# Kernel optimization log

Measured on AMD Instinct MI355X. Metric: run time of the kernel, lower is better.

Reference implementation:

```python
import jax, jax.numpy as jnp
import numpy as np

E, D, H, B, S = 16, 1024, 256, 4, 4096  # num_splats, model_dim, ff_dim//num_splats, batch, seq_len


def setup_inputs() -> dict:
    key = jax.random.key(0)
    ks = jax.random.split(key, 8)
    s = 0.02  # init scale for stability
    return {
        "x": jax.random.normal(ks[0], (B, S, D), dtype=jnp.float32),
        "splat_id": jax.random.randint(ks[1], (S,), 0, E, dtype=jnp.int32),
        "W1": jax.random.normal(ks[2], (E, D, H), dtype=jnp.float32) * s,
        "b1": jnp.zeros((E, H), dtype=jnp.float32),
        "W2": jax.random.normal(ks[3], (E, H, D), dtype=jnp.float32) * s,
        "b2": jnp.zeros((E, D), dtype=jnp.float32),
        "Wg1": jax.random.normal(ks[4], (D, D), dtype=jnp.float32) * s,
        "bg1": jnp.zeros((D,), dtype=jnp.float32),
        "Wg2": jax.random.normal(ks[5], (D, D), dtype=jnp.float32) * s,
        "bg2": jnp.zeros((D,), dtype=jnp.float32),
    }


def reference(x, splat_id, W1, b1, W2, b2, Wg1, bg1, Wg2, bg2):
    # Splat-aware dispatch: token s is processed by expert splat_id[s].
    # Equivalent vectorized form: run every expert's small MLP, mask at the
    # hidden layer by expert assignment, and sum over experts (each token is
    # assigned to exactly one expert, matching the gather->MLP->scatter loop).
    nE = W1.shape[0]
    onehot = (splat_id[None, :] == jnp.arange(nE, dtype=splat_id.dtype)[:, None]).astype(x.dtype)  # [E,S]
    # hidden: [E,B,S,H]
    h = jax.nn.gelu(jnp.einsum('bsd,edh->ebsh', x, W1) + b1[:, None, None, :], approximate=False)
    h = h * onehot[:, None, :, None]  # zero tokens not routed to expert e
    routed = jnp.einsum('ebsh,ehd->bsd', h, W2)  # [B,S,D]
    routed = routed + jnp.einsum('es,ed->sd', onehot, b2)[None, :, :]  # per-token expert bias
    # global aggregator MLP (torch GELU default = exact erf form)
    g = jax.nn.gelu(routed @ Wg1 + bg1, approximate=False)
    return g @ Wg2 + bg2
```

## Files before the change

### kernel.cpp

```cpp
#include <hip/hip_runtime.h>


#define DEV __device__ __forceinline__

typedef float f32x4 __attribute__((ext_vector_type(4)));
typedef short short8 __attribute__((ext_vector_type(8)));

DEV unsigned short f2bf(float f) {
  unsigned u = __float_as_uint(f);
  u += 0x7fffu + ((u >> 16) & 1u);
  return (unsigned short)(u >> 16);
}

DEV void gload16(const void* g, void* l) {
  __builtin_amdgcn_global_load_lds(
      (const __attribute__((address_space(1))) unsigned int*)g,
      (__attribute__((address_space(3))) unsigned int*)l, 16, 0, 0);
}

DEV float gelu_exact(float v) {
  return 0.5f * v * (1.0f + erff(v * 0.70710678118654752f));
}

__global__ __launch_bounds__(256) void prep_kernel(
    const float* __restrict__ W1, unsigned short* __restrict__ w1t,
    const float* __restrict__ W2, unsigned short* __restrict__ w2t,
    const float* __restrict__ Wg1, unsigned short* __restrict__ wg1t,
    const float* __restrict__ Wg2, unsigned short* __restrict__ wg2t) {
  __shared__ float tile[64][65];
  const int t = threadIdx.x;
  int id = (int)blockIdx.x;
  const float* in; unsigned short* out;
  int R, C, r0, c0; long base;
  if (id < 1024) {
    in = W1; out = w1t; R = 1024; C = 256;
    base = (long)(id >> 6) * 262144;
    r0 = ((id >> 2) & 15) * 64; c0 = (id & 3) * 64;
  } else if (id < 2048) {
    id -= 1024;
    in = W2; out = w2t; R = 256; C = 1024;
    base = (long)(id >> 6) * 262144;
    r0 = ((id >> 4) & 3) * 64; c0 = (id & 15) * 64;
  } else if (id < 2304) {
    id -= 2048;
    in = Wg1; out = wg1t; R = 1024; C = 1024; base = 0;
    r0 = (id >> 4) * 64; c0 = (id & 15) * 64;
  } else {
    id -= 2304;
    in = Wg2; out = wg2t; R = 1024; C = 1024; base = 0;
    r0 = (id >> 4) * 64; c0 = (id & 15) * 64;
  }
  const int cc = t & 63, rr = t >> 6;
#pragma unroll
  for (int i = 0; i < 16; i++) {
    int r = rr + i * 4;
    tile[r][cc] = in[base + (long)(r0 + r) * C + (c0 + cc)];
  }
  __syncthreads();
#pragma unroll
  for (int i = 0; i < 16; i++) {
    int c = rr + i * 4;
    out[base + (long)(c0 + c) * R + (r0 + cc)] = f2bf(tile[cc][c]);
  }
}

__global__ __launch_bounds__(256) void route_kernel(
    const int* __restrict__ sid, int S, int* __restrict__ offs, int* __restrict__ order,
    int* __restrict__ tileE, int* __restrict__ tileR, int* __restrict__ ntl,
    int* __restrict__ t64E, int* __restrict__ t64R, int* __restrict__ ntl64) {
  __shared__ int cnt[16], cur[16];
  const int t = threadIdx.x;
  if (t < 16) cnt[t] = 0;
  __syncthreads();
  for (int s = t; s < S; s += 256) atomicAdd(&cnt[sid[s]], 1);
  __syncthreads();
  if (t == 0) {
    int a = 0;
    for (int e = 0; e < 16; e++) { offs[e] = a; cur[e] = a; a += cnt[e]; }
    offs[16] = a;
    int nt = 0, n64 = 0;
    for (int e = 0; e < 16; e++) {
      const int rows = 4 * cnt[e];
      for (int r = 0; r < rows; r += 128) {
        tileE[nt] = e; tileR[nt] = 4 * offs[e] + r; nt++;
      }
      for (int r = 0; r < rows; r += 64) {
        t64E[n64] = e; t64R[n64] = 4 * offs[e] + r; n64++;
      }
    }
    ntl[0] = nt;
    ntl64[0] = n64;
  }
  __syncthreads();
  for (int s = t; s < S; s += 256) {
    int p = atomicAdd(&cur[sid[s]], 1);
    order[p] = s;
  }
}

__global__ __launch_bounds__(256, 4) void gemm_g1(
    const float* __restrict__ x,
    const unsigned short* __restrict__ w1t, const float* __restrict__ b1,
    unsigned short* __restrict__ hbuf,
    const int* __restrict__ order, const int* __restrict__ offs,
    const int* __restrict__ t64E, const int* __restrict__ t64R,
    const int* __restrict__ ntl64) {
  constexpr int S = 4096, D = 1024, H = 256;
  const int ti = (int)blockIdx.y;
  if (ti >= ntl64[0]) return;
  const int ntile = (int)blockIdx.x;
  const int t = (int)threadIdx.x;
  const int lane = t & 63;
  const int wn = t >> 6;

  const int e = t64E[ti];
  const int rowBase = t64R[ti];
  int Me = 4 * offs[e + 1] - rowBase;
  if (Me > 64) Me = 64;

  __shared__ __align__(16) unsigned short lA[64 * 64];
  __shared__ __align__(16) unsigned short lB[128 * 64];

  const float* xsrc[2];
  int aDst[2];
#pragma unroll
  for (int i = 0; i < 2; i++) {
    const int row = i * 32 + (t >> 3);
    const int koff = (((t & 7) * 16) ^ ((row & 7) << 4)) >> 1;
    const int rr = (row < Me) ? row : (Me - 1);
    const int g = rowBase + rr;
    xsrc[i] = x + ((long)(g & 3) * S + order[g >> 2]) * D + koff;
    aDst[i] = row * 64 + (t & 7) * 8;
  }
  const unsigned short* bSrc[4];
#pragma unroll
  for (int i = 0; i < 4; i++) {
    const int row = i * 32 + (t >> 3);
    bSrc[i] = w1t + (long)e * H * D + (long)(ntile * 128 + row) * D +
              ((((t & 7) * 16) ^ ((row & 7) << 4)) >> 1);
  }
  const int dstE = (t >> 3) * 64 + (t & 7) * 8;

  f32x4 acc[4][2] = {};
  float4 xv[2][2];
#pragma unroll
  for (int i = 0; i < 2; i++) {
    xv[i][0] = *(const float4*)(xsrc[i]);
    xv[i][1] = *(const float4*)(xsrc[i] + 4);
  }

  for (int kt = 0; kt < 16; kt++) {
    __syncthreads();
#pragma unroll
    for (int i = 0; i < 2; i++) {
      short8 av;
      av[0] = (short)f2bf(xv[i][0].x); av[1] = (short)f2bf(xv[i][0].y);
      av[2] = (short)f2bf(xv[i][0].z); av[3] = (short)f2bf(xv[i][0].w);
      av[4] = (short)f2bf(xv[i][1].x); av[5] = (short)f2bf(xv[i][1].y);
      av[6] = (short)f2bf(xv[i][1].z); av[7] = (short)f2bf(xv[i][1].w);
      *(short8*)(lA + aDst[i]) = av;
    }
#pragma unroll
    for (int i = 0; i < 4; i++)
      gload16(bSrc[i] + (kt << 6), lB + i * 2048 + dstE);
    if (kt < 15) {
#pragma unroll
      for (int i = 0; i < 2; i++) {
        xv[i][0] = *(const float4*)(xsrc[i] + (kt + 1) * 64);
        xv[i][1] = *(const float4*)(xsrc[i] + (kt + 1) * 64 + 4);
      }
    }
    __syncthreads();
#pragma unroll
    for (int kk = 0; kk < 2; kk++) {
      short8 aF[4], bF[2];
      const int kb = kk * 64 + ((lane >> 4) << 4);
#pragma unroll
      for (int mi = 0; mi < 4; mi++) {
        const int row = mi * 16 + (lane & 15);
        aF[mi] = *(const short8*)((const char*)lA + row * 128 + (kb ^ ((row & 7) << 4)));
      }
#pragma unroll
      for (int ni = 0; ni < 2; ni++) {
        const int row = wn * 32 + ni * 16 + (lane & 15);
        bF[ni] = *(const short8*)((const char*)lB + row * 128 + (kb ^ ((row & 7) << 4)));
      }
#pragma unroll
      for (int mi = 0; mi < 4; mi++)
#pragma unroll
        for (int ni = 0; ni < 2; ni++)
          acc[mi][ni] = __builtin_amdgcn_mfma_f32_16x16x32_bf16(aF[mi], bF[ni], acc[mi][ni], 0, 0, 0);
    }
  }

  float bc[2];
#pragma unroll
  for (int ni = 0; ni < 2; ni++)
    bc[ni] = b1[e * H + ntile * 128 + wn * 32 + ni * 16 + (lane & 15)];
#pragma unroll
  for (int mi = 0; mi < 4; mi++)
#pragma unroll
    for (int j = 0; j < 4; j++) {
      const int lrow = mi * 16 + ((lane >> 4) << 2) + j;
      if (lrow >= Me) continue;
      const long crow = rowBase + lrow;
#pragma unroll
      for (int ni = 0; ni < 2; ni++) {
        const float v = gelu_exact(acc[mi][ni][j] + bc[ni]);
        hbuf[crow * H + ntile * 128 + wn * 32 + ni * 16 + (lane & 15)] = f2bf(v);
      }
    }
}

__global__ __launch_bounds__(256) void gemm_g2(
    const unsigned short* __restrict__ A, const unsigned short* __restrict__ BT,
    const float* __restrict__ bias, unsigned short* __restrict__ Cout,
    int N, int K,
    const int* __restrict__ order, const int* __restrict__ offs,
    const int* __restrict__ tileE, const int* __restrict__ tileR,
    const int* __restrict__ ntl,
    int S, long btStride, int biasStride) {
  const int ti = (int)blockIdx.y;
  if (ti >= ntl[0]) return;
  const int t = (int)threadIdx.x;
  const int lane = t & 63;
  const int w = t >> 6;
  const int wm = w >> 1, wn = w & 1;
  const int tileN = (int)blockIdx.x;

  const int e = tileE[ti];
  const int rowBase = tileR[ti];
  int Me = 4 * offs[e + 1] - rowBase;
  if (Me > 128) Me = 128;
  const unsigned short* bt = BT + (long)e * btStride;
  const float* bs = bias + (long)e * biasStride;

  __shared__ __align__(16) unsigned short lA[128 * 64];
  __shared__ __align__(16) unsigned short lB[128 * 64];

  const unsigned short* aSrc[4];
  const unsigned short* bSrc[4];
  {
    const int q = t & 7;
#pragma unroll
    for (int i = 0; i < 4; i++) {
      const int row = i * 32 + (t >> 3);
      const int koff = ((q * 16) ^ ((row & 7) << 4)) >> 1;
      const int rr = (row < Me) ? row : (Me - 1);
      const int g = rowBase + rr;
      aSrc[i] = A + (long)g * K + koff;
      const int col = tileN * 128 + row;
      bSrc[i] = bt + (long)col * K + koff;
    }
  }

  f32x4 acc[4][4] = {};

  const int KT = K >> 6;
  for (int kt = 0; kt < KT; kt++) {
    __syncthreads();
#pragma unroll
    for (int i = 0; i < 4; i++) {
      gload16(aSrc[i] + (kt << 6), (void*)(lA + i * 2048 + w * 512));
      gload16(bSrc[i] + (kt << 6), (void*)(lB + i * 2048 + w * 512));
    }
    __syncthreads();
#pragma unroll
    for (int kk = 0; kk < 2; kk++) {
      short8 af[4], bfr[4];
      const int kbyte = kk * 64 + (lane >> 4) * 16;
#pragma unroll
      for (int mi = 0; mi < 4; mi++) {
        const int row = wm * 64 + mi * 16 + (lane & 15);
        const int off = row * 128 + (kbyte ^ ((row & 7) << 4));
        af[mi] = *(const short8*)((const char*)lA + off);
      }
#pragma unroll
      for (int ni = 0; ni < 4; ni++) {
        const int row = wn * 64 + ni * 16 + (lane & 15);
        const int off = row * 128 + (kbyte ^ ((row & 7) << 4));
        bfr[ni] = *(const short8*)((const char*)lB + off);
      }
#pragma unroll
      for (int mi = 0; mi < 4; mi++)
#pragma unroll
        for (int ni = 0; ni < 4; ni++)
          acc[mi][ni] = __builtin_amdgcn_mfma_f32_16x16x32_bf16(af[mi], bfr[ni], acc[mi][ni], 0, 0, 0);
    }
  }

  float bcol[4];
#pragma unroll
  for (int ni = 0; ni < 4; ni++)
    bcol[ni] = bs[tileN * 128 + wn * 64 + ni * 16 + (lane & 15)];

#pragma unroll
  for (int mi = 0; mi < 4; mi++) {
#pragma unroll
    for (int j = 0; j < 4; j++) {
      const int lrow = wm * 64 + mi * 16 + ((lane >> 4) * 4) + j;
      if (lrow >= Me) continue;
      const int g = rowBase + lrow;
      const long crow = (long)(g & 3) * S + order[g >> 2];
#pragma unroll
      for (int ni = 0; ni < 4; ni++) {
        const float v = acc[mi][ni][j] + bcol[ni];
        Cout[crow * (long)N + tileN * 128 + wn * 64 + ni * 16 + (lane & 15)] = f2bf(v);
      }
    }
  }
}

template <bool GELU, bool OUT_F32>
__global__ __launch_bounds__(256, 4) void gemm_dense128(
    const unsigned short* __restrict__ A, const unsigned short* __restrict__ BT,
    const float* __restrict__ bias, void* __restrict__ Cout,
    int N, int K, int ntiles) {
  const int t = (int)threadIdx.x;
  const int lane = t & 63;
  const int w = t >> 6;
  const int wm = w >> 1, wn = w & 1;

  const int cpx = (int)gridDim.x >> 3;
  const int swz = ((int)blockIdx.x & 7) * cpx + ((int)blockIdx.x >> 3);
  const int mtile = swz / ntiles, ntile = swz % ntiles;

  __shared__ __align__(16) unsigned short lA[128 * 64];
  __shared__ __align__(16) unsigned short lB[128 * 64];

  const unsigned short* aSrc[4];
  const unsigned short* bSrc[4];
  {
    const int q = t & 7;
#pragma unroll
    for (int i = 0; i < 4; i++) {
      const int row = i * 32 + (t >> 3);
      const int koff = ((q * 16) ^ ((row & 7) << 4)) >> 1;
      aSrc[i] = A + (long)(mtile * 128 + row) * K + koff;
      bSrc[i] = BT + (long)(ntile * 128 + row) * K + koff;
    }
  }

  f32x4 acc[4][4] = {};

  const int KT = K >> 6;
  for (int kt = 0; kt < KT; kt++) {
    __syncthreads();
#pragma unroll
    for (int i = 0; i < 4; i++) {
      gload16(aSrc[i] + (kt << 6), (void*)(lA + i * 2048 + w * 512));
      gload16(bSrc[i] + (kt << 6), (void*)(lB + i * 2048 + w * 512));
    }
    __syncthreads();
#pragma unroll
    for (int kk = 0; kk < 2; kk++) {
      short8 af[4], bfr[4];
      const int kbyte = kk * 64 + (lane >> 4) * 16;
#pragma unroll
      for (int mi = 0; mi < 4; mi++) {
        const int row = wm * 64 + mi * 16 + (lane & 15);
        const int off = row * 128 + (kbyte ^ ((row & 7) << 4));
        af[mi] = *(const short8*)((const char*)lA + off);
      }
#pragma unroll
      for (int ni = 0; ni < 4; ni++) {
        const int row = wn * 64 + ni * 16 + (lane & 15);
        const int off = row * 128 + (kbyte ^ ((row & 7) << 4));
        bfr[ni] = *(const short8*)((const char*)lB + off);
      }
#pragma unroll
      for (int mi = 0; mi < 4; mi++)
#pragma unroll
        for (int ni = 0; ni < 4; ni++)
          acc[mi][ni] = __builtin_amdgcn_mfma_f32_16x16x32_bf16(af[mi], bfr[ni], acc[mi][ni], 0, 0, 0);
    }
  }

  float bcol[4];
#pragma unroll
  for (int ni = 0; ni < 4; ni++)
    bcol[ni] = bias[ntile * 128 + wn * 64 + ni * 16 + (lane & 15)];

#pragma unroll
  for (int mi = 0; mi < 4; mi++) {
#pragma unroll
    for (int j = 0; j < 4; j++) {
      const long crow = mtile * 128 + wm * 64 + mi * 16 + ((lane >> 4) * 4) + j;
#pragma unroll
      for (int ni = 0; ni < 4; ni++) {
        float v = acc[mi][ni][j] + bcol[ni];
        if (GELU) v = gelu_exact(v);
        const long cidx = crow * (long)N + ntile * 128 + wn * 64 + ni * 16 + (lane & 15);
        if (OUT_F32) ((float*)Cout)[cidx] = v;
        else ((unsigned short*)Cout)[cidx] = f2bf(v);
      }
    }
  }
}

extern "C" void kernel_launch(void* const* d_in, const int* in_sizes, int n_in,
                              void* d_out, int out_size, void* d_ws, size_t ws_size,
                              hipStream_t stream) {
  const float* x   = (const float*)d_in[0];
  const int*   sid = (const int*)d_in[1];
  const float* W1  = (const float*)d_in[2];
  const float* b1  = (const float*)d_in[3];
  const float* W2  = (const float*)d_in[4];
  const float* b2  = (const float*)d_in[5];
  const float* Wg1 = (const float*)d_in[6];
  const float* bg1 = (const float*)d_in[7];
  const float* Wg2 = (const float*)d_in[8];
  const float* bg2 = (const float*)d_in[9];
  (void)in_sizes; (void)n_in; (void)out_size; (void)ws_size;

  constexpr int D = 1024, H = 256, S = 4096, B = 4;
  constexpr long NT = (long)B * S;

  char* ws = (char*)d_ws;
  unsigned short* gbuf = (unsigned short*)(ws);
  unsigned short* w1t  = (unsigned short*)(ws + 33554432);
  unsigned short* w2t  = (unsigned short*)(ws + 41943040);
  unsigned short* wg1t = (unsigned short*)(ws + 50331648);
  unsigned short* wg2t = (unsigned short*)(ws + 52428800);
  unsigned short* hbuf = (unsigned short*)(ws + 54525952);
  unsigned short* rout = (unsigned short*)(ws + 62914560);
  int* offs  = (int*)(ws + 96468992);
  int* order = (int*)(ws + 96469248);
  int* tileE = (int*)(ws + 96485632);
  int* tileR = (int*)(ws + 96486208);
  int* ntl   = (int*)(ws + 96486784);
  int* t64E  = (int*)(ws + 96487424);
  int* t64R  = (int*)(ws + 96488704);
  int* ntl64 = (int*)(ws + 96489984);

  prep_kernel<<<dim3(2560), 256, 0, stream>>>(W1, w1t, W2, w2t, Wg1, wg1t, Wg2, wg2t);
  route_kernel<<<1, 256, 0, stream>>>(sid, S, offs, order, tileE, tileR, ntl, t64E, t64R, ntl64);

  gemm_g1<<<dim3(H / 128, 272), 256, 0, stream>>>(
      x, w1t, b1, hbuf, order, offs, t64E, t64R, ntl64);
  gemm_g2<<<dim3(D / 128, 144), 256, 0, stream>>>(
      hbuf, w2t, b2, rout, D, H, order, offs, tileE, tileR, ntl, S, (long)D * H, D);
  gemm_dense128<true, false><<<dim3((unsigned)(NT / 128) * (D / 128)), 256, 0, stream>>>(
      rout, wg1t, bg1, gbuf, D, D, D / 128);
  gemm_dense128<false, true><<<dim3((unsigned)(NT / 128) * (D / 128)), 256, 0, stream>>>(
      gbuf, wg2t, bg2, d_out, D, D, D / 128);
}
```

Measured before the change: 181.3 us.

## Use 128-row tiles in expert GEMM1 with fp32 async LDS loads of x

Expert GEMM1 moves from 64x128 tiles to 128x128 tiles over a 2x2 wave grid, so each block reuses weight tiles across twice as many token rows and the grid has half as many row tiles. The gathered fp32 activations now go straight into LDS through async global_load_lds instead of through registers with an explicit bf16 convert-and-store. Conversion to bf16 happens while reading LDS fragments, using round-half-up rather than round-to-nearest-even. This doubles the A-tile LDS footprint and the accumulator registers (occupancy hint lowered to 3), and drops the register prefetch of the next x tile. Launch bounds on gemm_g2 and the launch order of the route and prep kernels also change.

```diff
diff --git a/kernel.cpp b/kernel.cpp
--- a/kernel.cpp
+++ b/kernel.cpp
@@ -20,6 +20,35 @@
 
 DEV float gelu_exact(float v) {
   return 0.5f * v * (1.0f + erff(v * 0.70710678118654752f));
+}
+
+__global__ __launch_bounds__(256) void route_kernel(
+    const int* __restrict__ sid, int S, int* __restrict__ offs, int* __restrict__ order,
+    int* __restrict__ tileE, int* __restrict__ tileR, int* __restrict__ ntl) {
+  __shared__ int cnt[16], cur[16];
+  const int t = threadIdx.x;
+  if (t < 16) cnt[t] = 0;
+  __syncthreads();
+  for (int s = t; s < S; s += 256) atomicAdd(&cnt[sid[s]], 1);
+  __syncthreads();
+  if (t == 0) {
+    int a = 0;
+    for (int e = 0; e < 16; e++) { offs[e] = a; cur[e] = a; a += cnt[e]; }
+    offs[16] = a;
+    int nt = 0;
+    for (int e = 0; e < 16; e++) {
+      const int rows = 4 * cnt[e];
+      for (int r = 0; r < rows; r += 128) {
+        tileE[nt] = e; tileR[nt] = 4 * offs[e] + r; nt++;
+      }
+    }
+    ntl[0] = nt;
+  }
+  __syncthreads();
+  for (int s = t; s < S; s += 256) {
+    int p = atomicAdd(&cur[sid[s]], 1);
+    order[p] = s;
+  }
 }
 
 __global__ __launch_bounds__(256) void prep_kernel(
@@ -64,74 +93,41 @@
   }
 }
 
-__global__ __launch_bounds__(256) void route_kernel(
-    const int* __restrict__ sid, int S, int* __restrict__ offs, int* __restrict__ order,
-    int* __restrict__ tileE, int* __restrict__ tileR, int* __restrict__ ntl,
-    int* __restrict__ t64E, int* __restrict__ t64R, int* __restrict__ ntl64) {
-  __shared__ int cnt[16], cur[16];
-  const int t = threadIdx.x;
-  if (t < 16) cnt[t] = 0;
-  __syncthreads();
-  for (int s = t; s < S; s += 256) atomicAdd(&cnt[sid[s]], 1);
-  __syncthreads();
-  if (t == 0) {
-    int a = 0;
-    for (int e = 0; e < 16; e++) { offs[e] = a; cur[e] = a; a += cnt[e]; }
-    offs[16] = a;
-    int nt = 0, n64 = 0;
-    for (int e = 0; e < 16; e++) {
-      const int rows = 4 * cnt[e];
-      for (int r = 0; r < rows; r += 128) {
-        tileE[nt] = e; tileR[nt] = 4 * offs[e] + r; nt++;
-      }
-      for (int r = 0; r < rows; r += 64) {
-        t64E[n64] = e; t64R[n64] = 4 * offs[e] + r; n64++;
-      }
-    }
-    ntl[0] = nt;
-    ntl64[0] = n64;
-  }
-  __syncthreads();
-  for (int s = t; s < S; s += 256) {
-    int p = atomicAdd(&cur[sid[s]], 1);
-    order[p] = s;
-  }
-}
-
-__global__ __launch_bounds__(256, 4) void gemm_g1(
+__global__ __launch_bounds__(256, 3) void gemm_g1f(
     const float* __restrict__ x,
     const unsigned short* __restrict__ w1t, const float* __restrict__ b1,
     unsigned short* __restrict__ hbuf,
     const int* __restrict__ order, const int* __restrict__ offs,
-    const int* __restrict__ t64E, const int* __restrict__ t64R,
-    const int* __restrict__ ntl64) {
+    const int* __restrict__ tileE, const int* __restrict__ tileR,
+    const int* __restrict__ ntl) {
   constexpr int S = 4096, D = 1024, H = 256;
   const int ti = (int)blockIdx.y;
-  if (ti >= ntl64[0]) return;
+  if (ti >= ntl[0]) return;
   const int ntile = (int)blockIdx.x;
   const int t = (int)threadIdx.x;
   const int lane = t & 63;
-  const int wn = t >> 6;
-
-  const int e = t64E[ti];
-  const int rowBase = t64R[ti];
+  const int w = t >> 6;
+  const int wm = w >> 1, wn = w & 1;
+
+  const int e = tileE[ti];
+  const int rowBase = tileR[ti];
   int Me = 4 * offs[e + 1] - rowBase;
-  if (Me > 64) Me = 64;
-
-  __shared__ __align__(16) unsigned short lA[64 * 64];
+  if (Me > 128) Me = 128;
+
+  __shared__ __align__(16) float lAf[128 * 64];
   __shared__ __align__(16) unsigned short lB[128 * 64];
 
-  const float* xsrc[2];
-  int aDst[2];
-#pragma unroll
-  for (int i = 0; i < 2; i++) {
-    const int row = i * 32 + (t >> 3);
-    const int koff = (((t & 7) * 16) ^ ((row & 7) << 4)) >> 1;
+  const float* aSrc[8];
+#pragma unroll
+  for (int i = 0; i < 8; i++) {
+    const int row = i * 16 + (t >> 4);
+    const int koffA = (((t & 15) * 16) ^ ((row & 7) << 5)) >> 2;
     const int rr = (row < Me) ? row : (Me - 1);
     const int g = rowBase + rr;
-    xsrc[i] = x + ((long)(g & 3) * S + order[g >> 2]) * D + koff;
-    aDst[i] = row * 64 + (t & 7) * 8;
-  }
+    aSrc[i] = x + ((long)(g & 3) * S + order[g >> 2]) * D + koffA;
+  }
+  const int dstA = (t >> 4) * 64 + (t & 15) * 4;
+
   const unsigned short* bSrc[4];
 #pragma unroll
   for (int i = 0; i < 4; i++) {
@@ -139,80 +135,72 @@
     bSrc[i] = w1t + (long)e * H * D + (long)(ntile * 128 + row) * D +
               ((((t & 7) * 16) ^ ((row & 7) << 4)) >> 1);
   }
-  const int dstE = (t >> 3) * 64 + (t & 7) * 8;
-
-  f32x4 acc[4][2] = {};
-  float4 xv[2][2];
-#pragma unroll
-  for (int i = 0; i < 2; i++) {
-    xv[i][0] = *(const float4*)(xsrc[i]);
-    xv[i][1] = *(const float4*)(xsrc[i] + 4);
-  }
+  const int dstB = (t >> 3) * 64 + (t & 7) * 8;
+
+  f32x4 acc[4][4] = {};
 
   for (int kt = 0; kt < 16; kt++) {
     __syncthreads();
 #pragma unroll
-    for (int i = 0; i < 2; i++) {
-      short8 av;
-      av[0] = (short)f2bf(xv[i][0].x); av[1] = (short)f2bf(xv[i][0].y);
-      av[2] = (short)f2bf(xv[i][0].z); av[3] = (short)f2bf(xv[i][0].w);
-      av[4] = (short)f2bf(xv[i][1].x); av[5] = (short)f2bf(xv[i][1].y);
-      av[6] = (short)f2bf(xv[i][1].z); av[7] = (short)f2bf(xv[i][1].w);
-      *(short8*)(lA + aDst[i]) = av;
-    }
+    for (int i = 0; i < 8; i++)
+      gload16(aSrc[i] + (kt << 6), lAf + i * 1024 + dstA);
 #pragma unroll
     for (int i = 0; i < 4; i++)
-      gload16(bSrc[i] + (kt << 6), lB + i * 2048 + dstE);
-    if (kt < 15) {
-#pragma unroll
-      for (int i = 0; i < 2; i++) {
-        xv[i][0] = *(const float4*)(xsrc[i] + (kt + 1) * 64);
-        xv[i][1] = *(const float4*)(xsrc[i] + (kt + 1) * 64 + 4);
-      }
-    }
+      gload16(bSrc[i] + (kt << 6), lB + i * 2048 + dstB);
     __syncthreads();
 #pragma unroll
     for (int kk = 0; kk < 2; kk++) {
-      short8 aF[4], bF[2];
-      const int kb = kk * 64 + ((lane >> 4) << 4);
+      short8 aF[4], bF[4];
+      const int kbA = kk * 128 + ((lane >> 4) << 5);
+      const int kbB = kk * 64 + ((lane >> 4) << 4);
 #pragma unroll
       for (int mi = 0; mi < 4; mi++) {
-        const int row = mi * 16 + (lane & 15);
-        aF[mi] = *(const short8*)((const char*)lA + row * 128 + (kb ^ ((row & 7) << 4)));
-      }
-#pragma unroll
-      for (int ni = 0; ni < 2; ni++) {
-        const int row = wn * 32 + ni * 16 + (lane & 15);
-        bF[ni] = *(const short8*)((const char*)lB + row * 128 + (kb ^ ((row & 7) << 4)));
+        const int row = wm * 64 + mi * 16 + (lane & 15);
+        const char* p = (const char*)lAf + row * 256 + (kbA ^ ((row & 7) << 5));
+        const f32x4 u0 = *(const f32x4*)p;
+        const f32x4 u1 = *(const f32x4*)(p + 16);
+        short8 af;
+#pragma unroll
+        for (int j = 0; j < 4; j++)
+          af[j] = (short)((__float_as_uint(u0[j]) + 0x8000u) >> 16);
+#pragma unroll
+        for (int j = 0; j < 4; j++)
+          af[4 + j] = (short)((__float_as_uint(u1[j]) + 0x8000u) >> 16);
+        aF[mi] = af;
+      }
+#pragma unroll
+      for (int ni = 0; ni < 4; ni++) {
+        const int row = wn * 64 + ni * 16 + (lane & 15);
+        bF[ni] = *(const short8*)((const char*)lB + row * 128 + (kbB ^ ((row & 7) << 4)));
       }
 #pragma unroll
       for (int mi = 0; mi < 4; mi++)
 #pragma unroll
-        for (int ni = 0; ni < 2; ni++)
+        for (int ni = 0; ni < 4; ni++)
           acc[mi][ni] = __builtin_amdgcn_mfma_f32_16x16x32_bf16(aF[mi], bF[ni], acc[mi][ni], 0, 0, 0);
     }
   }
 
-  float bc[2];
-#pragma unroll
-  for (int ni = 0; ni < 2; ni++)
-    bc[ni] = b1[e * H + ntile * 128 + wn * 32 + ni * 16 + (lane & 15)];
+  float bc[4];
+#pragma unroll
+  for (int ni = 0; ni < 4; ni++)
+    bc[ni] = b1[e * H + ntile * 128 + wn * 64 + ni * 16 + (lane & 15)];
 #pragma unroll
   for (int mi = 0; mi < 4; mi++)
 #pragma unroll
     for (int j = 0; j < 4; j++) {
-      const int lrow = mi * 16 + ((lane >> 4) << 2) + j;
+      const int lrow = wm * 64 + mi * 16 + ((lane >> 4) << 2) + j;
       if (lrow >= Me) continue;
       const long crow = rowBase + lrow;
 #pragma unroll
-      for (int ni = 0; ni < 2; ni++) {
+      for (int ni = 0; ni < 4; ni++) {
         const float v = gelu_exact(acc[mi][ni][j] + bc[ni]);
-        hbuf[crow * H + ntile * 128 + wn * 32 + ni * 16 + (lane & 15)] = f2bf(v);
-      }
-    }
-}
-
-__global__ __launch_bounds__(256) void gemm_g2(
+        hbuf[crow * H + ntile * 128 + wn * 64 + ni * 16 + (lane & 15)] = f2bf(v);
+      }
+    }
+}
+
+__global__ __launch_bounds__(256, 4) void gemm_g2(
     const unsigned short* __restrict__ A, const unsigned short* __restrict__ BT,
     const float* __restrict__ bias, unsigned short* __restrict__ Cout,
     int N, int K,
@@ -247,8 +235,7 @@
       const int row = i * 32 + (t >> 3);
       const int koff = ((q * 16) ^ ((row & 7) << 4)) >> 1;
       const int rr = (row < Me) ? row : (Me - 1);
-      const int g = rowBase + rr;
-      aSrc[i] = A + (long)g * K + koff;
+      aSrc[i] = A + (long)(rowBase + rr) * K + koff;
       const int col = tileN * 128 + row;
       bSrc[i] = bt + (long)col * K + koff;
     }
@@ -429,15 +416,12 @@
   int* tileE = (int*)(ws + 96485632);
   int* tileR = (int*)(ws + 96486208);
   int* ntl   = (int*)(ws + 96486784);
-  int* t64E  = (int*)(ws + 96487424);
-  int* t64R  = (int*)(ws + 96488704);
-  int* ntl64 = (int*)(ws + 96489984);
-
+
+  route_kernel<<<1, 256, 0, stream>>>(sid, S, offs, order, tileE, tileR, ntl);
   prep_kernel<<<dim3(2560), 256, 0, stream>>>(W1, w1t, W2, w2t, Wg1, wg1t, Wg2, wg2t);
-  route_kernel<<<1, 256, 0, stream>>>(sid, S, offs, order, tileE, tileR, ntl, t64E, t64R, ntl64);
-
-  gemm_g1<<<dim3(H / 128, 272), 256, 0, stream>>>(
-      x, w1t, b1, hbuf, order, offs, t64E, t64R, ntl64);
+
+  gemm_g1f<<<dim3(H / 128, 144), 256, 0, stream>>>(
+      x, w1t, b1, hbuf, order, offs, tileE, tileR, ntl);
   gemm_g2<<<dim3(D / 128, 144), 256, 0, stream>>>(
       hbuf, w2t, b2, rout, D, H, order, offs, tileE, tileR, ntl, S, (long)D * H, D);
   gemm_dense128<true, false><<<dim3((unsigned)(NT / 128) * (D / 128)), 256, 0, stream>>>(
```

After: 181.1 us. About the same (-0.1%).
